# Performance work log

Hardware: AMD Instinct MI355X
Metric: run time of the kernel (lower is better)

## Reference

```python
import jax, jax.numpy as jnp
import numpy as np

LN_EPS = 1e-5

def _layernorm(x, g, b):
    mu = x.mean(-1, keepdims=True)
    var = ((x - mu) ** 2).mean(-1, keepdims=True)
    return (x - mu) * jax.lax.rsqrt(var + LN_EPS) * g + b

def setup_inputs() -> dict:
    key = jax.random.key(0)
    ks = jax.random.split(key, 5)
    B, S, H, V = 1, 1024, 768, 50257
    return {
        "hidden_states": jax.random.normal(ks[0], (B, S, H), jnp.float32),
        "attention_mask": jnp.ones((B, S), jnp.int32),
        "alpha": jnp.float32(0.1),
        "ln_gamma": jnp.ones((H,), jnp.float32),
        "ln_beta": jnp.zeros((H,), jnp.float32),
        "W1": jax.random.normal(ks[1], (H, H), jnp.float32) * 0.02,
        "b1": jnp.zeros((H,), jnp.float32),
        "W2": jax.random.normal(ks[2], (H, H), jnp.float32) * 0.02,
        "b2": jnp.zeros((H,), jnp.float32),
        "lm_head_w": jax.random.normal(ks[3], (V, H), jnp.float32) * 0.02,
        "n_processors": 4,
        "k_steps": 4,
    }

def reference(hidden_states, attention_mask, alpha, ln_gamma, ln_beta,
              W1, b1, W2, b2, lm_head_w, n_processors, k_steps):
    P = int(n_processors)
    K = int(k_steps)
    mask = attention_mask.astype(hidden_states.dtype)[..., None]        # [B,S,1]
    # processor_states: [P,B,S,H] (all initialized to the same hidden state)
    states = jnp.broadcast_to(hidden_states[None], (P,) + hidden_states.shape)
    for _ in range(K):
        # eval mode: dropout=identity, no noise -> mutate == mask multiply
        mut = states * mask                                             # [P,B,S,H]
        if P > 1:
            # mean of other processors = (sum_all - self)/(P-1)
            observe = (mut.sum(0, keepdims=True) - mut) / (P - 1)
        else:
            observe = jnp.zeros_like(mut)
        merged = mut + alpha * observe
        normed = _layernorm(merged, ln_gamma, ln_beta)
        h = jax.nn.gelu(jnp.einsum('pbsh,ih->pbsi', normed, W1) + b1,
                        approximate=False)
        delta = jnp.einsum('pbsi,hi->pbsh', h, W2) + b2
        states = (mut + delta) * mask
    consensus = states.mean(0)                                          # [B,S,H]
    logits = jnp.einsum('bsh,vh->bsv', consensus, lm_head_w)            # [B,S,V]
    processor_logits = jnp.einsum('pbsh,vh->pbsv', states, lm_head_w)   # [P,B,S,V]
    return logits, processor_logits, states
```

## Files before the change

kernel.cpp:

```cpp
#include <hip/hip_runtime.h>
#include <hip/hip_bf16.h>
#include <math.h>

#define S_LEN 1024
#define HDIM  768
#define NPROC 4
#define VOCAB 50257
#define KSTEPS 4

typedef __attribute__((ext_vector_type(4))) float f32x4;
typedef __attribute__((ext_vector_type(8))) short bf16x8;
typedef __attribute__((ext_vector_type(4))) short short4v;

static __device__ __forceinline__ ushort f2bf(float f) {
  union { __hip_bfloat16 b; ushort u; } cv;
  cv.b = __float2bfloat16(f);
  return cv.u;
}

#define GLOAD16(gp, lp) __builtin_amdgcn_global_load_lds( \
    (const __attribute__((address_space(1))) unsigned int*)(gp), \
    (__attribute__((address_space(3))) unsigned int*)(lp), 16, 0, 0)

__global__ __launch_bounds__(256) void prep_weights(
    const float* __restrict__ lmw, const float* __restrict__ W1,
    const float* __restrict__ W2, ushort* __restrict__ lm_bf,
    ushort* __restrict__ w1_bf, ushort* __restrict__ w2_bf,
    const float* __restrict__ hidden, const int* __restrict__ mask,
    const float* __restrict__ alphap, const float* __restrict__ gamma,
    const float* __restrict__ beta, ushort* __restrict__ normed) {
  const int LM4 = VOCAB * HDIM / 4;
  const int W4  = HDIM * HDIM / 4;
  const int LMB = (LM4 + 255) / 256;
  const int WB  = (W4 + 255) / 256;
  const int bid = blockIdx.x;
  const int tid = threadIdx.x;
  __shared__ float rs_[4], rq_[4];
  if (bid < LMB + 2 * WB) {
    const float* in; ushort* out; int n4, i;
    if (bid < LMB)           { in = lmw; out = lm_bf; n4 = LM4; i = bid * 256 + tid; }
    else if (bid < LMB + WB) { in = W1;  out = w1_bf; n4 = W4;  i = (bid - LMB) * 256 + tid; }
    else                     { in = W2;  out = w2_bf; n4 = W4;  i = (bid - LMB - WB) * 256 + tid; }
    if (i >= n4) return;
    f32x4 v = ((const f32x4*)in)[i];
    short4v o;
#pragma unroll
    for (int j = 0; j < 4; j++) o[j] = (short)f2bf(v[j]);
    ((short4v*)out)[i] = o;
  } else {
    const int s = bid - (LMB + 2 * WB);
    const float mk = (float)mask[s];
    const float a1 = 1.0f + alphap[0];
    float merged[3];
    float lsum = 0.f, lsq = 0.f;
#pragma unroll
    for (int e = 0; e < 3; e++) {
      const int h = tid + e * 256;
      float mg = hidden[(size_t)s * HDIM + h] * mk * a1;
      merged[e] = mg;
      lsum += mg;
      lsq += mg * mg;
    }
#pragma unroll
    for (int off = 32; off > 0; off >>= 1) {
      lsum += __shfl_down(lsum, off, 64);
      lsq  += __shfl_down(lsq, off, 64);
    }
    const int wv = tid >> 6, ln = tid & 63;
    if (ln == 0) { rs_[wv] = lsum; rq_[wv] = lsq; }
    __syncthreads();
    const float ts = rs_[0] + rs_[1] + rs_[2] + rs_[3];
    const float tq = rq_[0] + rq_[1] + rq_[2] + rq_[3];
    const float mu = ts * (1.f / HDIM);
    const float var = tq * (1.f / HDIM) - mu * mu;
    const float rstd = rsqrtf(var + 1e-5f);
#pragma unroll
    for (int e = 0; e < 3; e++) {
      const int h = tid + e * 256;
      float nv = (merged[e] - mu) * rstd * gamma[h] + beta[h];
      normed[(size_t)s * HDIM + h] = f2bf(nv);
    }
  }
}

__global__ __launch_bounds__(256) void bcast_logits(
    const float* __restrict__ src, float* __restrict__ dst) {
  const size_t n4 = (size_t)S_LEN * VOCAB / 4;
  for (size_t i = (size_t)blockIdx.x * 256 + threadIdx.x; i < n4;
       i += (size_t)gridDim.x * 256) {
    f32x4 v = ((const f32x4*)src)[i];
#pragma unroll
    for (int p = 0; p < NPROC; p++)
      ((f32x4*)dst)[(size_t)p * n4 + i] = v;
  }
}

__global__ __launch_bounds__(256) void merge_ln_p1(
    const float* __restrict__ src, const int* __restrict__ mask,
    const float* __restrict__ alphap, const float* __restrict__ gamma,
    const float* __restrict__ beta, ushort* __restrict__ normed) {
  const int s = blockIdx.x;
  const int tid = threadIdx.x;
  const float mk = (float)mask[s];
  const float a1 = 1.0f + alphap[0];
  float merged[3];
  float lsum = 0.f, lsq = 0.f;
#pragma unroll
  for (int e = 0; e < 3; e++) {
    const int h = tid + e * 256;
    float mg = src[(size_t)s * HDIM + h] * mk * a1;
    merged[e] = mg;
    lsum += mg;
    lsq += mg * mg;
  }
#pragma unroll
  for (int off = 32; off > 0; off >>= 1) {
    lsum += __shfl_down(lsum, off, 64);
    lsq  += __shfl_down(lsq, off, 64);
  }
  __shared__ float rs_[4], rq_[4];
  const int wv = tid >> 6, ln = tid & 63;
  if (ln == 0) { rs_[wv] = lsum; rq_[wv] = lsq; }
  __syncthreads();
  const float ts = rs_[0] + rs_[1] + rs_[2] + rs_[3];
  const float tq = rq_[0] + rq_[1] + rq_[2] + rq_[3];
  const float mu = ts * (1.f / HDIM);
  const float var = tq * (1.f / HDIM) - mu * mu;
  const float rstd = rsqrtf(var + 1e-5f);
#pragma unroll
  for (int e = 0; e < 3; e++) {
    const int h = tid + e * 256;
    float nv = (merged[e] - mu) * rstd * gamma[h] + beta[h];
    normed[(size_t)s * HDIM + h] = f2bf(nv);
  }
}

template <int MODE>
__global__ __launch_bounds__(256, 4) void gemm_bt(
    const ushort* __restrict__ A, const ushort* __restrict__ B,
    const float* __restrict__ bias, ushort* __restrict__ out_bf,
    const float* __restrict__ src, float* __restrict__ dst,
    float* __restrict__ states, const int* __restrict__ mask, int nrowsB) {
  __shared__ __align__(16) ushort lsA[3][4096];
  __shared__ __align__(16) ushort lsB[3][2048];
  const int tid = threadIdx.x;
  const int bx = blockIdx.x;
  const int mt = bx & 7;
  const int nt = bx >> 3;
  const int wv = tid >> 6, lane = tid & 63;
  const int wm = wv >> 1, wn = wv & 1;
  const int g = lane >> 4, lr = lane & 15;

  f32x4 acc[4][2];
#pragma unroll
  for (int i = 0; i < 4; i++)
#pragma unroll
    for (int j = 0; j < 2; j++) acc[i][j] = (f32x4){0.f, 0.f, 0.f, 0.f};

  const int koff = (tid & 3) * 8;
  const int arow0 = mt * 128 + (tid >> 2);
  const ushort* gA0 = A + (size_t)arow0 * HDIM + koff;
  const ushort* gA1 = gA0 + (size_t)64 * HDIM;
  int brow = nt * 64 + (tid >> 2);
  if (MODE == 2 && brow >= nrowsB) brow = nrowsB - 1;
  const ushort* gB0 = B + (size_t)brow * HDIM + koff;
  const int dstl = (tid >> 2) * 32 + (tid & 3) * 8;

#define STAGE(kt, buf) do {                      \
    const int o_ = (kt) * 32;                    \
    GLOAD16(gA0 + o_, &lsA[buf][dstl]);          \
    GLOAD16(gA1 + o_, &lsA[buf][2048 + dstl]);   \
    GLOAD16(gB0 + o_, &lsB[buf][dstl]);          \
  } while (0)

  constexpr int NT = HDIM / 32;
  STAGE(0, 0);
  STAGE(1, 1);
  STAGE(2, 2);
  int cur = 0;
  for (int kt = 0; kt < NT; ++kt) {
    if (kt < NT - 2)       asm volatile("s_waitcnt vmcnt(6)" ::: "memory");
    else if (kt == NT - 2) asm volatile("s_waitcnt vmcnt(3)" ::: "memory");
    else                   asm volatile("s_waitcnt vmcnt(0)" ::: "memory");
    __builtin_amdgcn_s_barrier();
    __builtin_amdgcn_sched_barrier(0);
    bf16x8 af[4], bfr[2];
#pragma unroll
    for (int mi = 0; mi < 4; mi++)
      af[mi] = *(const bf16x8*)(&lsA[cur][(wm * 64 + mi * 16 + lr) * 32 + g * 8]);
#pragma unroll
    for (int ni = 0; ni < 2; ni++)
      bfr[ni] = *(const bf16x8*)(&lsB[cur][(wn * 32 + ni * 16 + lr) * 32 + g * 8]);
    asm volatile("s_waitcnt lgkmcnt(0)" ::: "memory");
    __builtin_amdgcn_sched_barrier(0);
    __builtin_amdgcn_s_setprio(1);
#pragma unroll
    for (int mi = 0; mi < 4; mi++)
#pragma unroll
      for (int ni = 0; ni < 2; ni++)
        acc[mi][ni] = __builtin_amdgcn_mfma_f32_16x16x32_bf16(af[mi], bfr[ni], acc[mi][ni], 0, 0, 0);
    __builtin_amdgcn_s_setprio(0);
    __builtin_amdgcn_s_barrier();
    __builtin_amdgcn_sched_barrier(0);
    if (kt + 3 < NT) STAGE(kt + 3, cur);
    cur = (cur == 2) ? 0 : cur + 1;
  }
#undef STAGE

#pragma unroll
  for (int mi = 0; mi < 4; mi++) {
    const int mrow = mt * 128 + wm * 64 + mi * 16 + g * 4;
#pragma unroll
    for (int ni = 0; ni < 2; ni++) {
      const int ncol = nt * 64 + wn * 32 + ni * 16 + lr;
      if (MODE == 0) {
        const float bv = bias[ncol];
#pragma unroll
        for (int j = 0; j < 4; j++) {
          float x = acc[mi][ni][j] + bv;
          float ge = 0.5f * x * (1.f + erff(x * 0.70710678118654752f));
          out_bf[(size_t)(mrow + j) * HDIM + ncol] = f2bf(ge);
        }
      } else if (MODE == 1) {
        const float bv = bias[ncol];
#pragma unroll
        for (int j = 0; j < 4; j++) {
          const int m = mrow + j;
          const float mk = (float)mask[m];
          const size_t idx = (size_t)m * HDIM + ncol;
          const float mut = src[idx] * mk;
          const float ns = (mut + acc[mi][ni][j] + bv) * mk;
          if (out_bf) {
            out_bf[idx] = f2bf(ns);
#pragma unroll
            for (int p = 0; p < NPROC; p++)
              states[(size_t)p * S_LEN * HDIM + idx] = ns;
          } else {
            dst[idx] = ns;
          }
        }
      } else {
        if (ncol < nrowsB) {
#pragma unroll
          for (int j = 0; j < 4; j++)
            dst[(size_t)(mrow + j) * VOCAB + ncol] = acc[mi][ni][j];
        }
      }
    }
  }
}

extern "C" void kernel_launch(void* const* d_in, const int* in_sizes, int n_in,
                              void* d_out, int out_size, void* d_ws, size_t ws_size,
                              hipStream_t stream) {
  const float* hidden = (const float*)d_in[0];
  const int*   mask   = (const int*)d_in[1];
  const float* alphap = (const float*)d_in[2];
  const float* gamma  = (const float*)d_in[3];
  const float* beta   = (const float*)d_in[4];
  const float* W1     = (const float*)d_in[5];
  const float* b1     = (const float*)d_in[6];
  const float* W2     = (const float*)d_in[7];
  const float* b2     = (const float*)d_in[8];
  const float* lmw    = (const float*)d_in[9];

  float* logits  = (float*)d_out;
  float* plogits = logits + (size_t)S_LEN * VOCAB;
  float* states  = plogits + (size_t)NPROC * S_LEN * VOCAB;

  uint8_t* ws = (uint8_t*)d_ws;
  ushort* lm_bf  = (ushort*)ws;
  ushort* w1_bf  = (ushort*)(ws + 77194752);
  ushort* w2_bf  = (ushort*)(ws + 78374400);
  ushort* nrm_bf = (ushort*)(ws + 79554048);
  ushort* h_bf   = (ushort*)(ws + 81126912);
  ushort* a_bf   = (ushort*)(ws + 82699776);
  float*  st1    = (float*) (ws + 84272640);
  if (ws_size < 87418368) return;

  const int LMB = (VOCAB * HDIM / 4 + 255) / 256, WB = (HDIM * HDIM / 4 + 255) / 256;
  prep_weights<<<LMB + 2 * WB + S_LEN, 256, 0, stream>>>(
      lmw, W1, W2, lm_bf, w1_bf, w2_bf, hidden, mask, alphap, gamma, beta, nrm_bf);

  for (int k = 0; k < KSTEPS; k++) {
    const float* src = (k == 0) ? hidden : st1;
    if (k > 0)
      merge_ln_p1<<<S_LEN, 256, 0, stream>>>(src, mask, alphap, gamma, beta, nrm_bf);
    gemm_bt<0><<<(HDIM / 64) * 8, 256, 0, stream>>>(
        nrm_bf, w1_bf, b1, h_bf, nullptr, nullptr, nullptr, mask, HDIM);
    gemm_bt<1><<<(HDIM / 64) * 8, 256, 0, stream>>>(
        h_bf, w2_bf, b2, (k == KSTEPS - 1) ? (ushort*)a_bf : nullptr,
        src, st1, states, mask, HDIM);
  }
  gemm_bt<2><<<((VOCAB + 63) / 64) * 8, 256, 0, stream>>>(
      a_bf, lm_bf, nullptr, nullptr, nullptr, logits, nullptr, nullptr, VOCAB);
  bcast_logits<<<2048, 256, 0, stream>>>(logits, plogits);
}
```

Before: 598.2 us.

## Replace LDS-staged LM-head GEMM with register-direct per-wave 64x64 tile kernel

Drops the LDS-pipelined 128x64 tiling for the large vocab projection. The new kernel has each wave compute an independent 64x64 output tile and load A and B fragments straight from global memory into registers, with no LDS and no barriers. This removes synchronisation and LDS staging overhead and relies on L2/cache reuse plus many waves to hide latency. The cost is uncoalesced-ish 16-byte strided global loads and no explicit prefetch pipeline, so the kernel depends on hardware latency hiding.

```diff
diff --git a/kernel.cpp b/kernel.cpp
--- a/kernel.cpp
+++ b/kernel.cpp
@@ -136,11 +136,11 @@
 }
 
 template <int MODE>
-__global__ __launch_bounds__(256, 4) void gemm_bt(
+__global__ __launch_bounds__(256, 4) void gemm_mlp(
     const ushort* __restrict__ A, const ushort* __restrict__ B,
     const float* __restrict__ bias, ushort* __restrict__ out_bf,
     const float* __restrict__ src, float* __restrict__ dst,
-    float* __restrict__ states, const int* __restrict__ mask, int nrowsB) {
+    float* __restrict__ states, const int* __restrict__ mask) {
   __shared__ __align__(16) ushort lsA[3][4096];
   __shared__ __align__(16) ushort lsB[3][2048];
   const int tid = threadIdx.x;
@@ -161,9 +161,7 @@
   const int arow0 = mt * 128 + (tid >> 2);
   const ushort* gA0 = A + (size_t)arow0 * HDIM + koff;
   const ushort* gA1 = gA0 + (size_t)64 * HDIM;
-  int brow = nt * 64 + (tid >> 2);
-  if (MODE == 2 && brow >= nrowsB) brow = nrowsB - 1;
-  const ushort* gB0 = B + (size_t)brow * HDIM + koff;
+  const ushort* gB0 = B + (size_t)(nt * 64 + (tid >> 2)) * HDIM + koff;
   const int dstl = (tid >> 2) * 32 + (tid & 3) * 8;
 
 #define STAGE(kt, buf) do {                      \
@@ -213,16 +211,15 @@
 #pragma unroll
     for (int ni = 0; ni < 2; ni++) {
       const int ncol = nt * 64 + wn * 32 + ni * 16 + lr;
+      const float bv = bias[ncol];
       if (MODE == 0) {
-        const float bv = bias[ncol];
 #pragma unroll
         for (int j = 0; j < 4; j++) {
           float x = acc[mi][ni][j] + bv;
           float ge = 0.5f * x * (1.f + erff(x * 0.70710678118654752f));
           out_bf[(size_t)(mrow + j) * HDIM + ncol] = f2bf(ge);
         }
-      } else if (MODE == 1) {
-        const float bv = bias[ncol];
+      } else {
 #pragma unroll
         for (int j = 0; j < 4; j++) {
           const int m = mrow + j;
@@ -239,12 +236,64 @@
             dst[idx] = ns;
           }
         }
-      } else {
-        if (ncol < nrowsB) {
-#pragma unroll
-          for (int j = 0; j < 4; j++)
-            dst[(size_t)(mrow + j) * VOCAB + ncol] = acc[mi][ni][j];
-        }
+      }
+    }
+  }
+}
+
+__global__ __launch_bounds__(256) void gemm_lm_tlp(
+    const ushort* __restrict__ A, const ushort* __restrict__ B,
+    float* __restrict__ logits) {
+  const int tid = threadIdx.x;
+  const int wv = tid >> 6, lane = tid & 63;
+  const int g = lane >> 4, lr = lane & 15;
+  const int bx = blockIdx.x;
+  const int mt = bx & 15;
+  const int ntg = bx >> 4;
+  const int nt = ntg * 4 + wv;
+  const int m0 = mt * 64;
+  const int n0 = nt * 64;
+
+  f32x4 acc[4][4];
+#pragma unroll
+  for (int i = 0; i < 4; i++)
+#pragma unroll
+    for (int j = 0; j < 4; j++) acc[i][j] = (f32x4){0.f, 0.f, 0.f, 0.f};
+
+  const ushort* Ab = A + (size_t)(m0 + lr) * HDIM + g * 8;
+  const ushort* Bb[4];
+#pragma unroll
+  for (int ni = 0; ni < 4; ni++) {
+    int r = n0 + ni * 16 + lr;
+    if (r >= VOCAB) r = VOCAB - 1;
+    Bb[ni] = B + (size_t)r * HDIM + g * 8;
+  }
+
+  for (int kt = 0; kt < HDIM / 32; ++kt) {
+    bf16x8 af[4], bfr[4];
+#pragma unroll
+    for (int mi = 0; mi < 4; mi++)
+      af[mi] = *(const bf16x8*)(Ab + (size_t)mi * 16 * HDIM + kt * 32);
+#pragma unroll
+    for (int ni = 0; ni < 4; ni++)
+      bfr[ni] = *(const bf16x8*)(Bb[ni] + kt * 32);
+#pragma unroll
+    for (int mi = 0; mi < 4; mi++)
+#pragma unroll
+      for (int ni = 0; ni < 4; ni++)
+        acc[mi][ni] = __builtin_amdgcn_mfma_f32_16x16x32_bf16(af[mi], bfr[ni], acc[mi][ni], 0, 0, 0);
+  }
+
+#pragma unroll
+  for (int mi = 0; mi < 4; mi++) {
+    const int row0 = m0 + mi * 16 + g * 4;
+#pragma unroll
+    for (int ni = 0; ni < 4; ni++) {
+      const int col = n0 + ni * 16 + lr;
+      if (col < VOCAB) {
+#pragma unroll
+        for (int j = 0; j < 4; j++)
+          logits[(size_t)(row0 + j) * VOCAB + col] = acc[mi][ni][j];
       }
     }
   }
@@ -286,13 +335,12 @@
     const float* src = (k == 0) ? hidden : st1;
     if (k > 0)
       merge_ln_p1<<<S_LEN, 256, 0, stream>>>(src, mask, alphap, gamma, beta, nrm_bf);
-    gemm_bt<0><<<(HDIM / 64) * 8, 256, 0, stream>>>(
-        nrm_bf, w1_bf, b1, h_bf, nullptr, nullptr, nullptr, mask, HDIM);
-    gemm_bt<1><<<(HDIM / 64) * 8, 256, 0, stream>>>(
+    gemm_mlp<0><<<(HDIM / 64) * 8, 256, 0, stream>>>(
+        nrm_bf, w1_bf, b1, h_bf, nullptr, nullptr, nullptr, mask);
+    gemm_mlp<1><<<(HDIM / 64) * 8, 256, 0, stream>>>(
         h_bf, w2_bf, b2, (k == KSTEPS - 1) ? (ushort*)a_bf : nullptr,
-        src, st1, states, mask, HDIM);
-  }
-  gemm_bt<2><<<((VOCAB + 63) / 64) * 8, 256, 0, stream>>>(
-      a_bf, lm_bf, nullptr, nullptr, nullptr, logits, nullptr, nullptr, VOCAB);
+        src, st1, states, mask);
+  }
+  gemm_lm_tlp<<<16 * 197, 256, 0, stream>>>(a_bf, lm_bf, logits);
   bcast_logits<<<2048, 256, 0, stream>>>(logits, plogits);
 }
```

New measurement: 725.2 us. +21.2%, slower.
